# Kernel optimization log

Hardware: AMD Instinct MI355X
Metric: run time of the kernel (lower is better)

The kernel has to match this reference:

```python
import jax, jax.numpy as jnp
import numpy as np

N = 50000          # nodes
E = 800000         # edges (avg degree 16)
T = 4              # edge types (edge_attr_dim)
H = 8              # heads
C1 = 16            # state_dim (per-head channels, layer 1)
C2 = 8             # out_dim  (per-head channels, layer 2)
D = 128            # node_attr_dim
NEG = -1e9         # masked-attention logit
LRELU_SLOPE = 0.2  # PyG GATConv default negative_slope


def setup_inputs() -> dict:
    key = jax.random.key(0)
    ks = jax.random.split(key, 12)
    x = jax.random.normal(ks[0], (N, D), jnp.float32)
    edge_src = jax.random.randint(ks[1], (E,), 0, N, jnp.int32)
    edge_dst = jax.random.randint(ks[2], (E,), 0, N, jnp.int32)
    edge_type = jax.random.randint(ks[3], (E,), 0, T, jnp.int32)
    W1 = jax.random.normal(ks[4], (T, D, H * C1), jnp.float32) * (1.0 / np.sqrt(D))
    a1_src = jax.random.normal(ks[5], (T, H, C1), jnp.float32) * 0.1
    a1_dst = jax.random.normal(ks[6], (T, H, C1), jnp.float32) * 0.1
    b1 = jnp.zeros((T, H * C1), jnp.float32)
    W2 = jax.random.normal(ks[7], (T, H * C1, H * C2), jnp.float32) * (1.0 / np.sqrt(H * C1))
    a2_src = jax.random.normal(ks[8], (T, H, C2), jnp.float32) * 0.1
    a2_dst = jax.random.normal(ks[9], (T, H, C2), jnp.float32) * 0.1
    b2 = jnp.zeros((T, H * C2), jnp.float32)
    return dict(x=x, edge_src=edge_src, edge_dst=edge_dst, edge_type=edge_type,
                W1=W1, a1_src=a1_src, a1_dst=a1_dst, b1=b1,
                W2=W2, a2_src=a2_src, a2_dst=a2_dst, b2=b2)


def gat_conv(x_in, W, a_src, a_dst, b, src, dst, mask, n):
    """One PyG-style GATConv (concat heads, eval mode) on masked edge list."""
    heads, c = a_src.shape
    h = (x_in @ W).reshape(n, heads, c)                       # [N,H,C]
    s_src = jnp.sum(h * a_src, axis=-1)                        # [N,H]
    s_dst = jnp.sum(h * a_dst, axis=-1)                        # [N,H]
    e = jax.nn.leaky_relu(s_src[src] + s_dst[dst], LRELU_SLOPE)  # [Et,H]
    e = jnp.where(mask[:, None], e, NEG)
    m = jax.ops.segment_max(e, dst, num_segments=n)            # [N,H]
    p = jnp.exp(e - m[dst]) * mask[:, None].astype(e.dtype)    # unnorm softmax
    denom = jax.ops.segment_sum(p, dst, num_segments=n)        # [N,H]
    msg = p[:, :, None] * h[src]                               # [Et,H,C]
    agg = jax.ops.segment_sum(msg, dst, num_segments=n)        # [N,H,C]
    out = agg / denom[:, :, None]
    return out.reshape(n, heads * c) + b


def reference(x, edge_src, edge_dst, edge_type, W1, a1_src, a1_dst, b1,
              W2, a2_src, a2_dst, b2):
    n = x.shape[0]
    loops = jnp.arange(n, dtype=edge_src.dtype)
    src = jnp.concatenate([edge_src, loops])   # self-loops appended (PyG default)
    dst = jnp.concatenate([edge_dst, loops])
    ones = jnp.ones((n,), bool)
    outs = []
    for t in range(T):
        mask = jnp.concatenate([edge_type == t, ones])
        h1 = gat_conv(x, W1[t], a1_src[t], a1_dst[t], b1[t], src, dst, mask, n)
        h1 = jax.nn.relu(h1)
        h2 = gat_conv(h1, W2[t], a2_src[t], a2_dst[t], b2[t], src, dst, mask, n)
        outs.append(h2)
    return jnp.concatenate(outs, axis=1)       # [N, T*H*C2]
```

## Files before the change

### kernel.cpp

```cpp
#include <hip/hip_runtime.h>
#include <cstddef>

constexpr int NN  = 50000;
constexpr int NE  = 800000;
constexpr int NT  = 4;
constexpr int NH  = 8;
constexpr int C1  = 16;
constexpr int C2  = 8;
constexpr int DD  = 128;
constexpr int HC1 = NH * C1;
constexpr int HC2 = NH * C2;
constexpr int CAP = 22;
constexpr int BSTRIDE = 48;
constexpr float SLOPE = 0.2f;

constexpr int G_ZERO  = 2344;
constexpr int G_CONVB = 3125;
constexpr int G_P1    = NT * 16384 / 256;
constexpr int G_P2    = NT * 8192 / 256;
constexpr int G_SCATF = 782;
constexpr int G_GEMM  = (NN + 63) / 64;
constexpr int G_GAT1  = NN / 16;
constexpr int G_GAT2  = (NN + 31) / 32;

using short8 = __attribute__((ext_vector_type(8))) short;
using f32x4  = __attribute__((ext_vector_type(4))) float;
typedef unsigned short u16;

__device__ __forceinline__ float lrelu(float x) { return x > 0.f ? x : SLOPE * x; }
__device__ __forceinline__ float bfl(unsigned u) { return __uint_as_float(u << 16); }
__device__ __forceinline__ float bfh(unsigned u) { return __uint_as_float(u & 0xffff0000u); }
__device__ __forceinline__ u16 f2bf(float f) {
    unsigned u = __float_as_uint(f);
    return (u16)((u + 0x7fffu + ((u >> 16) & 1u)) >> 16);
}
__device__ __forceinline__ float dot8(uint4 hv, const float* a) {
    return bfl(hv.x) * a[0] + bfh(hv.x) * a[1] + bfl(hv.y) * a[2] + bfh(hv.y) * a[3]
         + bfl(hv.z) * a[4] + bfh(hv.z) * a[5] + bfl(hv.w) * a[6] + bfh(hv.w) * a[7];
}

__device__ __forceinline__ void scatter4(int e0, const int* __restrict__ esrc,
        const int* __restrict__ edst, const int* __restrict__ etyp,
        unsigned* __restrict__ bkt, int tmin, int tmax) {
    int bk[4], src[4];
    bool v[4];
    #pragma unroll
    for (int k = 0; k < 4; ++k) {
        int i = e0 + k * 256;
        bk[k] = 0; src[k] = 0;
        v[k] = false;
        if (i < NE) {
            int ty = etyp[i];
            v[k] = (ty >= tmin) && (ty <= tmax);
            if (v[k]) { bk[k] = ty * NN + edst[i]; src[k] = esrc[i]; }
        }
    }
    int slot[4];
    #pragma unroll
    for (int k = 0; k < 4; ++k)
        if (v[k]) slot[k] = atomicAdd((int*)((char*)bkt + (size_t)bk[k] * BSTRIDE), 1);
    #pragma unroll
    for (int k = 0; k < 4; ++k)
        if (v[k] && slot[k] < CAP)
            ((u16*)((char*)bkt + (size_t)bk[k] * BSTRIDE))[2 + slot[k]] = (u16)src[k];
}

template<bool XB>
__global__ __launch_bounds__(256) void init_kernel(const float* __restrict__ x,
        u16* __restrict__ xb, const float* __restrict__ W1, u16* __restrict__ wp1,
        const float* __restrict__ W2, u16* __restrict__ wp2,
        unsigned* __restrict__ bkt) {
    const int b = blockIdx.x, tid = threadIdx.x;
    const int CB = XB ? G_CONVB : 0;
    if (b < G_ZERO) {
        int i = b * 256 + tid;
        if (i < 600000) reinterpret_cast<uint4*>(bkt)[i] = make_uint4(0, 0, 0, 0);
    } else if (XB && b < G_ZERO + CB) {
        int i = (b - G_ZERO) * 256 + tid;
        float4 f0 = reinterpret_cast<const float4*>(x)[2 * i];
        float4 f1 = reinterpret_cast<const float4*>(x)[2 * i + 1];
        uint4 o;
        o.x = (unsigned)f2bf(f0.x) | ((unsigned)f2bf(f0.y) << 16);
        o.y = (unsigned)f2bf(f0.z) | ((unsigned)f2bf(f0.w) << 16);
        o.z = (unsigned)f2bf(f1.x) | ((unsigned)f2bf(f1.y) << 16);
        o.w = (unsigned)f2bf(f1.z) | ((unsigned)f2bf(f1.w) << 16);
        reinterpret_cast<uint4*>(xb)[i] = o;
    } else if (b < G_ZERO + CB + G_P1) {
        int i = (b - G_ZERO - CB) * 256 + tid;
        int t = i >> 14, r = i & 16383;
        int ntl = r >> 11, ks = (r >> 9) & 3, lane = (r >> 3) & 63, j = r & 7;
        int col = ntl * 16 + (lane & 15);
        int k   = ks * 32 + (lane >> 4) * 8 + j;
        wp1[i] = f2bf(W1[((size_t)t * DD + k) * HC1 + col]);
    } else {
        int i = (b - G_ZERO - CB - G_P1) * 256 + tid;
        int t = i >> 13, r = i & 8191;
        int ntl = r >> 11, ks = (r >> 9) & 3, lane = (r >> 3) & 63, j = r & 7;
        int col = ntl * 16 + (lane & 15);
        int k   = ks * 32 + (lane >> 4) * 8 + j;
        wp2[i] = f2bf(W2[((size_t)t * HC1 + k) * HC2 + col]);
    }
}

template<bool XB>
__device__ __forceinline__ void gemm1_body(int bx, int tid, const float* __restrict__ x,
        const u16* __restrict__ xb, const u16* __restrict__ Wp, u16* __restrict__ h1w) {
    constexpr int NTILE = HC1 / 16;
    const int wave = tid >> 6;
    const int lane = tid & 63;
    const int q    = lane >> 4;
    const int c    = lane & 15;
    const int rowbase = bx * 64 + wave * 16;

    int arow = rowbase + c; if (arow >= NN) arow = NN - 1;
    short8 afrag[4];
    if (XB) {
        const u16* ap = xb + (size_t)arow * DD + q * 8;
        #pragma unroll
        for (int ks = 0; ks < 4; ++ks)
            afrag[ks] = *reinterpret_cast<const short8*>(ap + ks * 32);
    } else {
        const float* xp = x + (size_t)arow * DD + q * 8;
        #pragma unroll
        for (int ks = 0; ks < 4; ++ks) {
            float4 f0 = *reinterpret_cast<const float4*>(xp + ks * 32);
            float4 f1 = *reinterpret_cast<const float4*>(xp + ks * 32 + 4);
            short8 a;
            a[0] = (short)f2bf(f0.x); a[1] = (short)f2bf(f0.y);
            a[2] = (short)f2bf(f0.z); a[3] = (short)f2bf(f0.w);
            a[4] = (short)f2bf(f1.x); a[5] = (short)f2bf(f1.y);
            a[6] = (short)f2bf(f1.z); a[7] = (short)f2bf(f1.w);
            afrag[ks] = a;
        }
    }

    f32x4 acc[NTILE];
    #pragma unroll
    for (int ntl = 0; ntl < NTILE; ++ntl) acc[ntl] = (f32x4){0.f, 0.f, 0.f, 0.f};
    const short8* wp = reinterpret_cast<const short8*>(Wp) + lane;
    #pragma unroll
    for (int ntl = 0; ntl < NTILE; ++ntl)
        #pragma unroll
        for (int ks = 0; ks < 4; ++ks) {
            short8 b = wp[(ntl * 4 + ks) * 64];
            acc[ntl] = __builtin_amdgcn_mfma_f32_16x16x32_bf16(afrag[ks], b, acc[ntl], 0, 0, 0);
        }

    #pragma unroll
    for (int ntl = 0; ntl < NTILE; ++ntl)
        #pragma unroll
        for (int reg = 0; reg < 4; ++reg) {
            int row = rowbase + q * 4 + reg;
            if (row < NN) h1w[(size_t)row * HC1 + ntl * 16 + c] = f2bf(acc[ntl][reg]);
        }
}

template<bool XB>
__global__ __launch_bounds__(256) void scatgemm_kernel(
        const int* __restrict__ esrc, const int* __restrict__ edst,
        const int* __restrict__ etyp, unsigned* __restrict__ bkt,
        const float* __restrict__ x, const u16* __restrict__ xb,
        const u16* __restrict__ wp1a, u16* __restrict__ h1a,
        const u16* __restrict__ wp1b, u16* __restrict__ h1b) {
    const int b = blockIdx.x, tid = threadIdx.x;
    if (b < G_SCATF) scatter4(b * 1024 + tid, esrc, edst, etyp, bkt, 0, 0);
    else if (b < G_SCATF + G_GEMM) gemm1_body<XB>(b - G_SCATF, tid, x, xb, wp1a, h1a);
    else gemm1_body<XB>(b - G_SCATF - G_GEMM, tid, x, xb, wp1b, h1b);
}

template<int TPN, bool SPLIT>
__device__ __forceinline__ void gather_body(const unsigned* __restrict__ bkt, int bk,
        int q, const float* asr, float sdn, const uint4* __restrict__ h4,
        float& den, float acc[8]) {
    const uint2* bp = reinterpret_cast<const uint2*>((const char*)bkt + (size_t)bk * BSTRIDE);
    unsigned w[12];
    #pragma unroll
    for (int i = 0; i < 6; ++i) { uint2 u = bp[i]; w[2 * i] = u.x; w[2 * i + 1] = u.y; }
    int deg = (int)w[0]; if (deg > CAP) deg = CAP;
    #pragma unroll
    for (int c = 0; c < 6; ++c) {
        if (c * 4 >= deg) break;
        unsigned lo = w[1 + 2 * c];
        unsigned hi = (c < 5) ? w[2 + 2 * c] : 0u;
        int sv[4] = {(int)(lo & 0xffff), (int)(lo >> 16),
                     (int)(hi & 0xffff), (int)(hi >> 16)};
        #pragma unroll
        for (int j = 0; j < 4; ++j) {
            if (c * 4 + j < deg) {
                int sn = sv[j];
                uint4 hv = h4[(size_t)sn * TPN + q];
                float d = dot8(hv, asr);
                if (SPLIT) d += __shfl_xor(d, 1);
                float pp = __expf(lrelu(d + sdn));
                den += pp;
                acc[0] += pp * bfl(hv.x); acc[1] += pp * bfh(hv.x);
                acc[2] += pp * bfl(hv.y); acc[3] += pp * bfh(hv.y);
                acc[4] += pp * bfl(hv.z); acc[5] += pp * bfh(hv.z);
                acc[6] += pp * bfl(hv.w); acc[7] += pp * bfh(hv.w);
            }
        }
    }
}

__device__ __forceinline__ void g1g2_body(int bx, int tid, const unsigned* __restrict__ bkt,
        int t, const u16* __restrict__ h1r, const float* __restrict__ a1s_t,
        const float* __restrict__ a1d_t, const float* __restrict__ b1t,
        const u16* __restrict__ wp2t, u16* __restrict__ h2w) {
    __shared__ u16 lt[16][136];
    const int node0 = bx * 16;
    const int nl    = tid >> 4;
    const int node  = node0 + nl;
    const int q     = tid & 15;
    const int head  = q >> 1;
    const int bk    = t * NN + node;
    const uint4* __restrict__ h4 = reinterpret_cast<const uint4*>(h1r);

    float asr[8], adr[8];
    #pragma unroll
    for (int i = 0; i < 8; ++i) {
        asr[i] = a1s_t[head * C1 + (q & 1) * 8 + i];
        adr[i] = a1d_t[head * C1 + (q & 1) * 8 + i];
    }

    uint4 hv = h4[(size_t)node * 16 + q];
    float ds = dot8(hv, asr); ds += __shfl_xor(ds, 1);
    float dd = dot8(hv, adr); dd += __shfl_xor(dd, 1);
    const float sdn = dd;

    float p = __expf(lrelu(ds + sdn));
    float den = p;
    float acc[8];
    acc[0] = p * bfl(hv.x); acc[1] = p * bfh(hv.x);
    acc[2] = p * bfl(hv.y); acc[3] = p * bfh(hv.y);
    acc[4] = p * bfl(hv.z); acc[5] = p * bfh(hv.z);
    acc[6] = p * bfl(hv.w); acc[7] = p * bfh(hv.w);
    gather_body<16, true>(bkt, bk, q, asr, sdn, h4, den, acc);

    float inv = 1.f / den;
    uint4 ov;
    {
        float o[8];
        #pragma unroll
        for (int i = 0; i < 8; ++i)
            o[i] = fmaxf(acc[i] * inv + b1t[q * 8 + i], 0.f);
        ov.x = (unsigned)f2bf(o[0]) | ((unsigned)f2bf(o[1]) << 16);
        ov.y = (unsigned)f2bf(o[2]) | ((unsigned)f2bf(o[3]) << 16);
        ov.z = (unsigned)f2bf(o[4]) | ((unsigned)f2bf(o[5]) << 16);
        ov.w = (unsigned)f2bf(o[6]) | ((unsigned)f2bf(o[7]) << 16);
    }
    *reinterpret_cast<uint4*>(&lt[nl][q * 8]) = ov;
    __syncthreads();

    const int wave = tid >> 6;
    const int lane = tid & 63;
    const int quad = lane >> 4;
    const int c    = lane & 15;
    short8 af[4];
    #pragma unroll
    for (int ks = 0; ks < 4; ++ks)
        af[ks] = *reinterpret_cast<const short8*>(&lt[c][ks * 32 + quad * 8]);
    f32x4 cacc = (f32x4){0.f, 0.f, 0.f, 0.f};
    const short8* wp = reinterpret_cast<const short8*>(wp2t) + lane;
    #pragma unroll
    for (int ks = 0; ks < 4; ++ks)
        cacc = __builtin_amdgcn_mfma_f32_16x16x32_bf16(af[ks], wp[(wave * 4 + ks) * 64], cacc, 0, 0, 0);

    const int col = wave * 16 + c;
    #pragma unroll
    for (int reg = 0; reg < 4; ++reg) {
        int row = node0 + quad * 4 + reg;
        h2w[(size_t)row * HC2 + col] = f2bf(cacc[reg]);
    }
}

__device__ __forceinline__ void gat2_body(int bx, int tid, const unsigned* __restrict__ bkt,
        int t, const u16* __restrict__ h2r, const float* __restrict__ a2s_t,
        const float* __restrict__ a2d_t, const float* __restrict__ b2t,
        float* __restrict__ out) {
    const int node = bx * 32 + (tid >> 3);
    if (node >= NN) return;
    const int q    = tid & 7;
    const int head = q;
    const int bk   = t * NN + node;
    const uint4* __restrict__ h4 = reinterpret_cast<const uint4*>(h2r);

    float asr[8], adr[8];
    #pragma unroll
    for (int i = 0; i < 8; ++i) {
        asr[i] = a2s_t[head * C2 + i];
        adr[i] = a2d_t[head * C2 + i];
    }

    uint4 hv = h4[(size_t)node * 8 + q];
    const float sdn = dot8(hv, adr);
    float p = __expf(lrelu(dot8(hv, asr) + sdn));
    float den = p;
    float acc[8];
    acc[0] = p * bfl(hv.x); acc[1] = p * bfh(hv.x);
    acc[2] = p * bfl(hv.y); acc[3] = p * bfh(hv.y);
    acc[4] = p * bfl(hv.z); acc[5] = p * bfh(hv.z);
    acc[6] = p * bfl(hv.w); acc[7] = p * bfh(hv.w);
    gather_body<8, false>(bkt, bk, q, asr, sdn, h4, den, acc);

    float inv = 1.f / den;
    float o[8];
    #pragma unroll
    for (int i = 0; i < 8; ++i) o[i] = acc[i] * inv + b2t[q * 8 + i];
    float* op = out + (size_t)node * (NT * HC2) + t * HC2 + q * 8;
    reinterpret_cast<float4*>(op)[0] = make_float4(o[0], o[1], o[2], o[3]);
    reinterpret_cast<float4*>(op)[1] = make_float4(o[4], o[5], o[6], o[7]);
}

template<bool XB>
__global__ __launch_bounds__(256) void mega_kernel(
        int nscat, int ngemm, int ng1,
        const int* __restrict__ esrc, const int* __restrict__ edst,
        const int* __restrict__ etyp, unsigned* __restrict__ bkt,
        int t1, const u16* __restrict__ h1r, const float* __restrict__ a1s_t,
        const float* __restrict__ a1d_t, const float* __restrict__ b1t,
        const u16* __restrict__ wp2t, u16* __restrict__ h2w,
        int t2, const u16* __restrict__ h2r, const float* __restrict__ a2s_t,
        const float* __restrict__ a2d_t, const float* __restrict__ b2t,
        float* __restrict__ out,
        const float* __restrict__ x, const u16* __restrict__ xb,
        const u16* __restrict__ wp1n, u16* __restrict__ h1w) {
    const int b = blockIdx.x, tid = threadIdx.x;
    if (b < nscat) {
        scatter4(b * 1024 + tid, esrc, edst, etyp, bkt, 1, 3);
    } else if (b < nscat + ngemm) {
        gemm1_body<XB>(b - nscat, tid, x, xb, wp1n, h1w);
    } else if (b < nscat + ngemm + ng1) {
        g1g2_body(b - nscat - ngemm, tid, bkt, t1, h1r, a1s_t, a1d_t, b1t, wp2t, h2w);
    } else {
        gat2_body(b - nscat - ngemm - ng1, tid, bkt, t2, h2r, a2s_t, a2d_t, b2t, out);
    }
}

template<bool XB>
static void run_pipeline(const float* x, const int* esrc, const int* edst,
        const int* etyp, const float* W1, const float* a1s, const float* a1d,
        const float* b1, const float* W2, const float* a2s, const float* a2d,
        const float* b2, float* out, char* base, hipStream_t stream) {
    size_t off = 0;
    u16* xb = nullptr;
    if (XB) { xb = (u16*)base; off += 12800000; }
    u16* h1d[2] = {(u16*)(base + off), (u16*)(base + off + 12800000)};
    off += 25600000;
    u16* h2d[2] = {(u16*)(base + off), (u16*)(base + off + 6400000)};
    off += 12800000;
    unsigned* bkt = (unsigned*)(base + off); off += 9600000;
    u16* wp1 = (u16*)(base + off); off += 131072;
    u16* wp2 = (u16*)(base + off);

    dim3 blk(256);
    int g_init = G_ZERO + (XB ? G_CONVB : 0) + G_P1 + G_P2;

    hipLaunchKernelGGL((init_kernel<XB>), dim3(g_init), blk, 0, stream,
                       x, xb, W1, wp1, W2, wp2, bkt);
    hipLaunchKernelGGL((scatgemm_kernel<XB>), dim3(G_SCATF + 2 * G_GEMM), blk, 0, stream,
                       esrc, edst, etyp, bkt, x, xb,
                       wp1, h1d[0], wp1 + 16384, h1d[1]);

    for (int t = 0; t < 5; ++t) {
        int nscat = (t == 0) ? G_SCATF : 0;
        int ngemm = (t == 1 || t == 2) ? G_GEMM : 0;
        int ng1   = (t < 4) ? G_GAT1 : 0;
        int ngat2 = (t >= 1) ? G_GAT2 : 0;
        int grid  = nscat + ngemm + ng1 + ngat2;
        int tm = (t < 4) ? t : 3;
        int tg = (t == 1 || t == 2) ? t + 1 : 0;
        int t2 = (t >= 1) ? t - 1 : 0;
        hipLaunchKernelGGL((mega_kernel<XB>), dim3(grid), blk, 0, stream,
                           nscat, ngemm, ng1, esrc, edst, etyp, bkt,
                           tm, h1d[tm & 1], a1s + tm * NH * C1, a1d + tm * NH * C1,
                           b1 + tm * HC1, wp2 + (size_t)tm * 8192, h2d[tm & 1],
                           t2, h2d[t2 & 1], a2s + t2 * NH * C2, a2d + t2 * NH * C2,
                           b2 + t2 * HC2, out,
                           x, xb, wp1 + (size_t)tg * 16384, h1d[tg & 1]);
    }
}

extern "C" void kernel_launch(void* const* d_in, const int* in_sizes, int n_in,
                              void* d_out, int out_size, void* d_ws, size_t ws_size,
                              hipStream_t stream) {
    const float* x    = (const float*)d_in[0];
    const int*   esrc = (const int*)d_in[1];
    const int*   edst = (const int*)d_in[2];
    const int*   etyp = (const int*)d_in[3];
    const float* W1   = (const float*)d_in[4];
    const float* a1s  = (const float*)d_in[5];
    const float* a1d  = (const float*)d_in[6];
    const float* b1   = (const float*)d_in[7];
    const float* W2   = (const float*)d_in[8];
    const float* a2s  = (const float*)d_in[9];
    const float* a2d  = (const float*)d_in[10];
    const float* b2   = (const float*)d_in[11];
    float* out = (float*)d_out;
    char* base = (char*)d_ws;

    if (ws_size >= 61000000)
        run_pipeline<true>(x, esrc, edst, etyp, W1, a1s, a1d, b1,
                           W2, a2s, a2d, b2, out, base, stream);
    else
        run_pipeline<false>(x, esrc, edst, etyp, W1, a1s, a1d, b1,
                            W2, a2s, a2d, b2, out, base, stream);
}
```

Measured before the change: 284.3 us.

## Store layer-1 features as int8 with per-row-per-head scales

The layer-1 GEMM output is quantized to int8 with one scale per node per head, computed by a shuffle max reduction across lanes. The gather stage then reads 8-byte int8 chunks plus a scale instead of 16-byte bf16 chunks and dequantizes in registers. This halves the bytes of the random-access neighbor gathers, which dominate the layer-1 aggregation. The cost is lower precision, some extra ALU work for dequantization, and a small extra scale array read on each gather.

```diff
diff --git a/kernel.cpp b/kernel.cpp
--- a/kernel.cpp
+++ b/kernel.cpp
@@ -26,6 +26,7 @@
 using short8 = __attribute__((ext_vector_type(8))) short;
 using f32x4  = __attribute__((ext_vector_type(4))) float;
 typedef unsigned short u16;
+typedef unsigned char  u8;
 
 __device__ __forceinline__ float lrelu(float x) { return x > 0.f ? x : SLOPE * x; }
 __device__ __forceinline__ float bfl(unsigned u) { return __uint_as_float(u << 16); }
@@ -33,6 +34,21 @@
 __device__ __forceinline__ u16 f2bf(float f) {
     unsigned u = __float_as_uint(f);
     return (u16)((u + 0x7fffu + ((u >> 16) & 1u)) >> 16);
+}
+__device__ __forceinline__ void deci8(uint2 v, float sc, float f[8]) {
+    int w0 = (int)v.x, w1 = (int)v.y;
+    f[0] = (float)((w0 << 24) >> 24) * sc;
+    f[1] = (float)((w0 << 16) >> 24) * sc;
+    f[2] = (float)((w0 <<  8) >> 24) * sc;
+    f[3] = (float)( w0        >> 24) * sc;
+    f[4] = (float)((w1 << 24) >> 24) * sc;
+    f[5] = (float)((w1 << 16) >> 24) * sc;
+    f[6] = (float)((w1 <<  8) >> 24) * sc;
+    f[7] = (float)( w1        >> 24) * sc;
+}
+__device__ __forceinline__ float dotf(const float h[8], const float* a) {
+    return h[0]*a[0] + h[1]*a[1] + h[2]*a[2] + h[3]*a[3]
+         + h[4]*a[4] + h[5]*a[5] + h[6]*a[6] + h[7]*a[7];
 }
 __device__ __forceinline__ float dot8(uint4 hv, const float* a) {
     return bfl(hv.x) * a[0] + bfh(hv.x) * a[1] + bfl(hv.y) * a[2] + bfh(hv.y) * a[3]
@@ -104,7 +120,8 @@
 
 template<bool XB>
 __device__ __forceinline__ void gemm1_body(int bx, int tid, const float* __restrict__ x,
-        const u16* __restrict__ xb, const u16* __restrict__ Wp, u16* __restrict__ h1w) {
+        const u16* __restrict__ xb, const u16* __restrict__ Wp,
+        u8* __restrict__ h1w, float* __restrict__ scw) {
     constexpr int NTILE = HC1 / 16;
     const int wave = tid >> 6;
     const int lane = tid & 63;
@@ -146,13 +163,41 @@
             acc[ntl] = __builtin_amdgcn_mfma_f32_16x16x32_bf16(afrag[ks], b, acc[ntl], 0, 0, 0);
         }
 
+    float mx[NTILE][4];
+    #pragma unroll
+    for (int ntl = 0; ntl < NTILE; ++ntl)
+        #pragma unroll
+        for (int reg = 0; reg < 4; ++reg) mx[ntl][reg] = fabsf(acc[ntl][reg]);
+    #pragma unroll
+    for (int m = 1; m < 16; m <<= 1)
+        #pragma unroll
+        for (int ntl = 0; ntl < NTILE; ++ntl)
+            #pragma unroll
+            for (int reg = 0; reg < 4; ++reg)
+                mx[ntl][reg] = fmaxf(mx[ntl][reg], __shfl_xor(mx[ntl][reg], m));
+
     #pragma unroll
     for (int ntl = 0; ntl < NTILE; ++ntl)
         #pragma unroll
         for (int reg = 0; reg < 4; ++reg) {
             int row = rowbase + q * 4 + reg;
-            if (row < NN) h1w[(size_t)row * HC1 + ntl * 16 + c] = f2bf(acc[ntl][reg]);
-        }
+            if (row < NN) {
+                float m = mx[ntl][reg];
+                float rs = m > 0.f ? 127.f / m : 0.f;
+                int iv = __float2int_rn(acc[ntl][reg] * rs);
+                h1w[(size_t)row * HC1 + ntl * 16 + c] = (u8)(char)iv;
+            }
+        }
+    {
+        int reg = c >> 2, hp = c & 3;
+        int row = rowbase + q * 4 + reg;
+        if (row < NN) {
+            float2 s;
+            s.x = mx[2 * hp][reg] * (1.f / 127.f);
+            s.y = mx[2 * hp + 1][reg] * (1.f / 127.f);
+            reinterpret_cast<float2*>(scw)[(size_t)row * 4 + hp] = s;
+        }
+    }
 }
 
 template<bool XB>
@@ -160,18 +205,18 @@
         const int* __restrict__ esrc, const int* __restrict__ edst,
         const int* __restrict__ etyp, unsigned* __restrict__ bkt,
         const float* __restrict__ x, const u16* __restrict__ xb,
-        const u16* __restrict__ wp1a, u16* __restrict__ h1a,
-        const u16* __restrict__ wp1b, u16* __restrict__ h1b) {
+        const u16* __restrict__ wp1a, u8* __restrict__ h1a, float* __restrict__ sca,
+        const u16* __restrict__ wp1b, u8* __restrict__ h1b, float* __restrict__ scb) {
     const int b = blockIdx.x, tid = threadIdx.x;
     if (b < G_SCATF) scatter4(b * 1024 + tid, esrc, edst, etyp, bkt, 0, 0);
-    else if (b < G_SCATF + G_GEMM) gemm1_body<XB>(b - G_SCATF, tid, x, xb, wp1a, h1a);
-    else gemm1_body<XB>(b - G_SCATF - G_GEMM, tid, x, xb, wp1b, h1b);
-}
-
-template<int TPN, bool SPLIT>
+    else if (b < G_SCATF + G_GEMM) gemm1_body<XB>(b - G_SCATF, tid, x, xb, wp1a, h1a, sca);
+    else gemm1_body<XB>(b - G_SCATF - G_GEMM, tid, x, xb, wp1b, h1b, scb);
+}
+
+template<int TPN, bool SPLIT, bool I8>
 __device__ __forceinline__ void gather_body(const unsigned* __restrict__ bkt, int bk,
-        int q, const float* asr, float sdn, const uint4* __restrict__ h4,
-        float& den, float acc[8]) {
+        int q, const float* asr, float sdn, const void* __restrict__ hbase,
+        const float* __restrict__ scp, float& den, float acc[8]) {
     const uint2* bp = reinterpret_cast<const uint2*>((const char*)bkt + (size_t)bk * BSTRIDE);
     unsigned w[12];
     #pragma unroll
@@ -188,24 +233,34 @@
         for (int j = 0; j < 4; ++j) {
             if (c * 4 + j < deg) {
                 int sn = sv[j];
-                uint4 hv = h4[(size_t)sn * TPN + q];
-                float d = dot8(hv, asr);
+                float hf[8];
+                if constexpr (I8) {
+                    uint2 hv = reinterpret_cast<const uint2*>(hbase)[(size_t)sn * TPN + q];
+                    float sc = scp[(size_t)sn * 8 + (q >> 1)];
+                    deci8(hv, sc, hf);
+                } else {
+                    uint4 hv = reinterpret_cast<const uint4*>(hbase)[(size_t)sn * TPN + q];
+                    hf[0] = bfl(hv.x); hf[1] = bfh(hv.x);
+                    hf[2] = bfl(hv.y); hf[3] = bfh(hv.y);
+                    hf[4] = bfl(hv.z); hf[5] = bfh(hv.z);
+                    hf[6] = bfl(hv.w); hf[7] = bfh(hv.w);
+                }
+                float d = dotf(hf, asr);
                 if (SPLIT) d += __shfl_xor(d, 1);
                 float pp = __expf(lrelu(d + sdn));
                 den += pp;
-                acc[0] += pp * bfl(hv.x); acc[1] += pp * bfh(hv.x);
-                acc[2] += pp * bfl(hv.y); acc[3] += pp * bfh(hv.y);
-                acc[4] += pp * bfl(hv.z); acc[5] += pp * bfh(hv.z);
-                acc[6] += pp * bfl(hv.w); acc[7] += pp * bfh(hv.w);
+                #pragma unroll
+                for (int i = 0; i < 8; ++i) acc[i] += pp * hf[i];
             }
         }
     }
 }
 
 __device__ __forceinline__ void g1g2_body(int bx, int tid, const unsigned* __restrict__ bkt,
-        int t, const u16* __restrict__ h1r, const float* __restrict__ a1s_t,
-        const float* __restrict__ a1d_t, const float* __restrict__ b1t,
-        const u16* __restrict__ wp2t, u16* __restrict__ h2w) {
+        int t, const u8* __restrict__ h1r, const float* __restrict__ sc1r,
+        const float* __restrict__ a1s_t, const float* __restrict__ a1d_t,
+        const float* __restrict__ b1t, const u16* __restrict__ wp2t,
+        u16* __restrict__ h2w) {
     __shared__ u16 lt[16][136];
     const int node0 = bx * 16;
     const int nl    = tid >> 4;
@@ -213,7 +268,6 @@
     const int q     = tid & 15;
     const int head  = q >> 1;
     const int bk    = t * NN + node;
-    const uint4* __restrict__ h4 = reinterpret_cast<const uint4*>(h1r);
 
     float asr[8], adr[8];
     #pragma unroll
@@ -222,19 +276,20 @@
         adr[i] = a1d_t[head * C1 + (q & 1) * 8 + i];
     }
 
-    uint4 hv = h4[(size_t)node * 16 + q];
-    float ds = dot8(hv, asr); ds += __shfl_xor(ds, 1);
-    float dd = dot8(hv, adr); dd += __shfl_xor(dd, 1);
+    uint2 hv = reinterpret_cast<const uint2*>(h1r)[(size_t)node * 16 + q];
+    float scn = sc1r[(size_t)node * 8 + head];
+    float hs[8];
+    deci8(hv, scn, hs);
+    float ds = dotf(hs, asr); ds += __shfl_xor(ds, 1);
+    float dd = dotf(hs, adr); dd += __shfl_xor(dd, 1);
     const float sdn = dd;
 
     float p = __expf(lrelu(ds + sdn));
     float den = p;
     float acc[8];
-    acc[0] = p * bfl(hv.x); acc[1] = p * bfh(hv.x);
-    acc[2] = p * bfl(hv.y); acc[3] = p * bfh(hv.y);
-    acc[4] = p * bfl(hv.z); acc[5] = p * bfh(hv.z);
-    acc[6] = p * bfl(hv.w); acc[7] = p * bfh(hv.w);
-    gather_body<16, true>(bkt, bk, q, asr, sdn, h4, den, acc);
+    #pragma unroll
+    for (int i = 0; i < 8; ++i) acc[i] = p * hs[i];
+    gather_body<16, true, true>(bkt, bk, q, asr, sdn, h1r, sc1r, den, acc);
 
     float inv = 1.f / den;
     uint4 ov;
@@ -300,7 +355,7 @@
     acc[2] = p * bfl(hv.y); acc[3] = p * bfh(hv.y);
     acc[4] = p * bfl(hv.z); acc[5] = p * bfh(hv.z);
     acc[6] = p * bfl(hv.w); acc[7] = p * bfh(hv.w);
-    gather_body<8, false>(bkt, bk, q, asr, sdn, h4, den, acc);
+    gather_body<8, false, false>(bkt, bk, q, asr, sdn, h2r, nullptr, den, acc);
 
     float inv = 1.f / den;
     float o[8];
@@ -316,21 +371,22 @@
         int nscat, int ngemm, int ng1,
         const int* __restrict__ esrc, const int* __restrict__ edst,
         const int* __restrict__ etyp, unsigned* __restrict__ bkt,
-        int t1, const u16* __restrict__ h1r, const float* __restrict__ a1s_t,
-        const float* __restrict__ a1d_t, const float* __restrict__ b1t,
-        const u16* __restrict__ wp2t, u16* __restrict__ h2w,
+        int t1, const u8* __restrict__ h1r, const float* __restrict__ sc1r,
+        const float* __restrict__ a1s_t, const float* __restrict__ a1d_t,
+        const float* __restrict__ b1t, const u16* __restrict__ wp2t,
+        u16* __restrict__ h2w,
         int t2, const u16* __restrict__ h2r, const float* __restrict__ a2s_t,
         const float* __restrict__ a2d_t, const float* __restrict__ b2t,
         float* __restrict__ out,
         const float* __restrict__ x, const u16* __restrict__ xb,
-        const u16* __restrict__ wp1n, u16* __restrict__ h1w) {
+        const u16* __restrict__ wp1n, u8* __restrict__ h1w, float* __restrict__ scw) {
     const int b = blockIdx.x, tid = threadIdx.x;
     if (b < nscat) {
         scatter4(b * 1024 + tid, esrc, edst, etyp, bkt, 1, 3);
     } else if (b < nscat + ngemm) {
-        gemm1_body<XB>(b - nscat, tid, x, xb, wp1n, h1w);
+        gemm1_body<XB>(b - nscat, tid, x, xb, wp1n, h1w, scw);
     } else if (b < nscat + ngemm + ng1) {
-        g1g2_body(b - nscat - ngemm, tid, bkt, t1, h1r, a1s_t, a1d_t, b1t, wp2t, h2w);
+        g1g2_body(b - nscat - ngemm, tid, bkt, t1, h1r, sc1r, a1s_t, a1d_t, b1t, wp2t, h2w);
     } else {
         gat2_body(b - nscat - ngemm - ng1, tid, bkt, t2, h2r, a2s_t, a2d_t, b2t, out);
     }
@@ -344,8 +400,10 @@
     size_t off = 0;
     u16* xb = nullptr;
     if (XB) { xb = (u16*)base; off += 12800000; }
-    u16* h1d[2] = {(u16*)(base + off), (u16*)(base + off + 12800000)};
-    off += 25600000;
+    u8* h1d[2] = {(u8*)(base + off), (u8*)(base + off + 6400000)};
+    off += 12800000;
+    float* sc1d[2] = {(float*)(base + off), (float*)(base + off + 1600000)};
+    off += 3200000;
     u16* h2d[2] = {(u16*)(base + off), (u16*)(base + off + 6400000)};
     off += 12800000;
     unsigned* bkt = (unsigned*)(base + off); off += 9600000;
@@ -359,7 +417,7 @@
                        x, xb, W1, wp1, W2, wp2, bkt);
     hipLaunchKernelGGL((scatgemm_kernel<XB>), dim3(G_SCATF + 2 * G_GEMM), blk, 0, stream,
                        esrc, edst, etyp, bkt, x, xb,
-                       wp1, h1d[0], wp1 + 16384, h1d[1]);
+                       wp1, h1d[0], sc1d[0], wp1 + 16384, h1d[1], sc1d[1]);
 
     for (int t = 0; t < 5; ++t) {
         int nscat = (t == 0) ? G_SCATF : 0;
@@ -372,11 +430,12 @@
         int t2 = (t >= 1) ? t - 1 : 0;
         hipLaunchKernelGGL((mega_kernel<XB>), dim3(grid), blk, 0, stream,
                            nscat, ngemm, ng1, esrc, edst, etyp, bkt,
-                           tm, h1d[tm & 1], a1s + tm * NH * C1, a1d + tm * NH * C1,
+                           tm, h1d[tm & 1], sc1d[tm & 1],
+                           a1s + tm * NH * C1, a1d + tm * NH * C1,
                            b1 + tm * HC1, wp2 + (size_t)tm * 8192, h2d[tm & 1],
                            t2, h2d[t2 & 1], a2s + t2 * NH * C2, a2d + t2 * NH * C2,
                            b2 + t2 * HC2, out,
-                           x, xb, wp1 + (size_t)tg * 16384, h1d[tg & 1]);
+                           x, xb, wp1 + (size_t)tg * 16384, h1d[tg & 1], sc1d[tg & 1]);
     }
 }
 
@@ -398,7 +457,7 @@
     float* out = (float*)d_out;
     char* base = (char*)d_ws;
 
-    if (ws_size >= 61000000)
+    if (ws_size >= 52000000)
         run_pipeline<true>(x, esrc, edst, etyp, W1, a1s, a1d, b1,
                            W2, a2s, a2d, b2, out, base, stream);
     else
```

After: 333.2 us. +17.2%, slower.
